# Kernel optimization log

Hardware: AMD Instinct MI355X
Metric: run time of the kernel (lower is better)

The kernel has to match this reference:

```python
import jax, jax.numpy as jnp
import numpy as np

B, L, D_MODEL = 2, 1024, 1024
N_LAYERS = 2
D_INNER = 2 * D_MODEL          # expand = 2
D_STATE = 16
D_CONV = 4
DT_RANK = (D_MODEL + 15) // 16  # ceil(d_model/16) = 64
INIT_SCALE = 0.02


def setup_inputs() -> dict:
    key = jax.random.key(0)
    ks = jax.random.split(key, 8)
    f32 = jnp.float32
    dt_init = float(np.log(np.expm1(0.01)))  # softplus^-1(0.01), standard mamba dt bias init
    return {
        "x": jax.random.normal(ks[0], (B, L, D_MODEL), f32),
        "W_in": jax.random.normal(ks[1], (N_LAYERS, 2 * D_INNER, D_MODEL), f32) * INIT_SCALE,
        "conv_w": jax.random.normal(ks[2], (N_LAYERS, D_INNER, D_CONV), f32) * INIT_SCALE,
        "conv_b": jnp.zeros((N_LAYERS, D_INNER), f32),
        "W_x": jax.random.normal(ks[3], (N_LAYERS, DT_RANK + 2 * D_STATE, D_INNER), f32) * INIT_SCALE,
        "W_dt": jax.random.normal(ks[4], (N_LAYERS, D_INNER, DT_RANK), f32) * INIT_SCALE,
        "b_dt": jnp.full((N_LAYERS, D_INNER), dt_init, f32),
        "A_log": jnp.tile(jnp.log(jnp.arange(1, D_STATE + 1, dtype=f32)), (N_LAYERS, D_INNER, 1)),
        "D": jnp.ones((N_LAYERS, D_INNER), f32),
        "W_out": jax.random.normal(ks[5], (N_LAYERS, D_MODEL, D_INNER), f32) * INIT_SCALE,
    }


def _silu(x):
    return x * jax.nn.sigmoid(x)


def _causal_conv1d(u, w, b):
    # u: [B, L, D_INNER], w: [D_INNER, D_CONV] depthwise, b: [D_INNER]
    ut = jnp.pad(jnp.transpose(u, (0, 2, 1)), ((0, 0), (0, 0), (D_CONV - 1, 0)))
    y = jax.lax.conv_general_dilated(
        ut, w[:, None, :], window_strides=(1,), padding='VALID',
        feature_group_count=D_INNER, dimension_numbers=('NCH', 'OIH', 'NCH'))
    return jnp.transpose(y + b[None, :, None], (0, 2, 1))


def _selective_scan(u, dt, A, Bm, Cm, Dvec):
    # u, dt: [B, L, D_INNER]; A: [D_INNER, N]; Bm, Cm: [B, L, N]; Dvec: [D_INNER]
    dA = jnp.exp(dt[..., None] * A)                        # [B,L,Din,N]
    dBu = dt[..., None] * Bm[:, :, None, :] * u[..., None]  # [B,L,Din,N]

    def step(h, xs):
        dA_t, dBu_t, C_t = xs                              # [B,Din,N],[B,Din,N],[B,N]
        h = dA_t * h + dBu_t
        y = jnp.einsum('bdn,bn->bd', h, C_t)
        return h, y

    h0 = jnp.zeros((u.shape[0], D_INNER, D_STATE), u.dtype)
    _, ys = jax.lax.scan(step, h0, (jnp.swapaxes(dA, 0, 1),
                                    jnp.swapaxes(dBu, 0, 1),
                                    jnp.swapaxes(Cm, 0, 1)))
    return jnp.swapaxes(ys, 0, 1) + u * Dvec               # [B,L,Din]


def _mamba_layer(x, W_in, conv_w, conv_b, W_x, W_dt, b_dt, A_log, Dvec, W_out):
    xz = jnp.einsum('bld,ed->ble', x, W_in)                # [B,L,2*Din]
    u, z = jnp.split(xz, 2, axis=-1)
    u = _silu(_causal_conv1d(u, conv_w, conv_b))
    x_dbl = jnp.einsum('bld,rd->blr', u, W_x)              # [B,L,dt_rank+2N]
    dt, Bm, Cm = jnp.split(x_dbl, [DT_RANK, DT_RANK + D_STATE], axis=-1)
    dt = jax.nn.softplus(jnp.einsum('blr,dr->bld', dt, W_dt) + b_dt)
    A = -jnp.exp(A_log)
    y = _selective_scan(u, dt, A, Bm, Cm, Dvec)
    y = y * _silu(z)
    return jnp.einsum('bld,od->blo', y, W_out)


def reference(x, W_in, conv_w, conv_b, W_x, W_dt, b_dt, A_log, D, W_out):
    residual = x
    h = x
    for i in range(N_LAYERS):
        h = _mamba_layer(h, W_in[i], conv_w[i], conv_b[i], W_x[i],
                         W_dt[i], b_dt[i], A_log[i], D[i], W_out[i])
    return h + residual
```

## Files before the change

### kernel.cpp

```cpp
#include <hip/hip_runtime.h>
#include <hip/hip_bf16.h>
#include <math.h>

#define B_ 2
#define L_ 1024
#define DM 1024
#define DIN 2048
#define DS 16
#define DTR 64
#define CHL 32
#define NCH 32

typedef __attribute__((ext_vector_type(8))) short bf16x8;
typedef __attribute__((ext_vector_type(8))) unsigned short u16x8;
typedef __attribute__((ext_vector_type(4))) unsigned short u16x4;
typedef __attribute__((ext_vector_type(4))) float f32x4;
typedef unsigned short ushort_t;
typedef unsigned int uint_t;

__device__ __forceinline__ float sigmoidf_(float x) { return 1.f / (1.f + __expf(-x)); }
__device__ __forceinline__ ushort_t f2b(float f) {
    uint_t b = __float_as_uint(f);
    return (ushort_t)((b + 0x7FFFu + ((b >> 16) & 1u)) >> 16);
}
__device__ __forceinline__ float b2f(ushort_t u) {
    return __uint_as_float(((uint_t)u) << 16);
}

__global__ __launch_bounds__(256) void f2b_all_k(
    const float* __restrict__ s0, ushort_t* __restrict__ d0, int n0,
    const float* __restrict__ s1, ushort_t* __restrict__ d1, int n1,
    const float* __restrict__ s2, ushort_t* __restrict__ d2, int n2,
    const float* __restrict__ s3, ushort_t* __restrict__ d3, int n3,
    const float* __restrict__ s4, ushort_t* __restrict__ d4, int n4)
{
    int i = (blockIdx.x * 256 + threadIdx.x) * 4;
    const float* s; ushort_t* d;
    if (i < n0) { s = s0; d = d0; }
    else { i -= n0;
    if (i < n1) { s = s1; d = d1; }
    else { i -= n1;
    if (i < n2) { s = s2; d = d2; }
    else { i -= n2;
    if (i < n3) { s = s3; d = d3; }
    else { i -= n3;
    if (i < n4) { s = s4; d = d4; }
    else return; }}}}
    float4 v = *(const float4*)(s + i);
    u16x4 o;
    o[0] = f2b(v.x); o[1] = f2b(v.y); o[2] = f2b(v.z); o[3] = f2b(v.w);
    *(u16x4*)(d + i) = o;
}

__device__ __forceinline__ int xcd_swz(int wgid, int nwg) {
    int cpx = nwg >> 3;
    return (wgid & 7) * cpx + (wgid >> 3);
}

__global__ __launch_bounds__(256) void mgemm_in(const ushort_t* __restrict__ A,
    const ushort_t* __restrict__ Bt, ushort_t* __restrict__ Cb,
    int M, int N, int K, int lda, int ldb)
{
    __shared__ ushort_t sA[2][128 * 32];
    __shared__ ushort_t sB[2][128 * 32];
    const int tid = threadIdx.x;
    const int lane = tid & 63, wv = tid >> 6;
    const int wm = wv >> 1, wn = wv & 1;
    const int swz = xcd_swz(blockIdx.y * gridDim.x + blockIdx.x, gridDim.x * gridDim.y);
    const int m0 = (swz / gridDim.x) * 128, n0 = (swz % gridDim.x) * 128;
    const int sr = tid >> 2;
    const int sc = (tid & 3) * 8;
    f32x4 acc[4][4] = {};

#pragma unroll
    for (int j = 0; j < 2; ++j) {
        int ra = sr + j * 64;
        __builtin_amdgcn_global_load_lds(
            (const uint_t*)(A + (size_t)(m0 + ra) * lda + sc),
            (uint_t*)(sA[0] + ra * 32 + sc), 16, 0, 0);
        __builtin_amdgcn_global_load_lds(
            (const uint_t*)(Bt + (size_t)(n0 + ra) * ldb + sc),
            (uint_t*)(sB[0] + ra * 32 + sc), 16, 0, 0);
    }
    __syncthreads();
    int cur = 0;
    for (int k0 = 0; k0 < K; k0 += 32) {
        if (k0 + 32 < K) {
            int nxt = cur ^ 1;
#pragma unroll
            for (int j = 0; j < 2; ++j) {
                int ra = sr + j * 64;
                __builtin_amdgcn_global_load_lds(
                    (const uint_t*)(A + (size_t)(m0 + ra) * lda + k0 + 32 + sc),
                    (uint_t*)(sA[nxt] + ra * 32 + sc), 16, 0, 0);
                __builtin_amdgcn_global_load_lds(
                    (const uint_t*)(Bt + (size_t)(n0 + ra) * ldb + k0 + 32 + sc),
                    (uint_t*)(sB[nxt] + ra * 32 + sc), 16, 0, 0);
            }
        }
        bf16x8 af[4], bfr[4];
#pragma unroll
        for (int i = 0; i < 4; ++i) {
            af[i]  = *(const bf16x8*)(sA[cur] + (wm * 64 + i * 16 + (lane & 15)) * 32 + (lane >> 4) * 8);
            bfr[i] = *(const bf16x8*)(sB[cur] + (wn * 64 + i * 16 + (lane & 15)) * 32 + (lane >> 4) * 8);
        }
#pragma unroll
        for (int i = 0; i < 4; ++i)
#pragma unroll
            for (int jj = 0; jj < 4; ++jj)
                acc[i][jj] = __builtin_amdgcn_mfma_f32_16x16x32_bf16(af[i], bfr[jj], acc[i][jj], 0, 0, 0);
        __syncthreads();
        cur ^= 1;
    }

    const int cr = (lane >> 4) * 4, cc = lane & 15;
#pragma unroll
    for (int i = 0; i < 4; ++i) {
        int mrow = m0 + wm * 64 + i * 16 + cr;
#pragma unroll
        for (int jj = 0; jj < 4; ++jj) {
            int ncol = n0 + wn * 64 + jj * 16 + cc;
#pragma unroll
            for (int r = 0; r < 4; ++r)
                Cb[(size_t)(mrow + r) * N + ncol] = f2b(acc[i][jj][r]);
        }
    }
}

__global__ __launch_bounds__(256) void mgemm_sk(const ushort_t* __restrict__ A,
    const ushort_t* __restrict__ Bt, float* __restrict__ P,
    int M, int N, int Kslice, int lda, int ldb)
{
    __shared__ ushort_t sA[2][128 * 32];
    __shared__ ushort_t sB[2][128 * 32];
    const int tid = threadIdx.x;
    const int lane = tid & 63, wv = tid >> 6;
    const int wm = wv >> 1, wn = wv & 1;
    const int m0 = blockIdx.y * 128;
    const int kbase = blockIdx.z * Kslice;
    const int sr = tid >> 2;
    const int sc = (tid & 3) * 8;
    f32x4 acc[4][4] = {};

#pragma unroll
    for (int j = 0; j < 2; ++j) {
        int ra = sr + j * 64;
        __builtin_amdgcn_global_load_lds(
            (const uint_t*)(A + (size_t)(m0 + ra) * lda + kbase + sc),
            (uint_t*)(sA[0] + ra * 32 + sc), 16, 0, 0);
        int gb = ra; if (gb >= N) gb = N - 1;
        __builtin_amdgcn_global_load_lds(
            (const uint_t*)(Bt + (size_t)gb * ldb + kbase + sc),
            (uint_t*)(sB[0] + ra * 32 + sc), 16, 0, 0);
    }
    __syncthreads();
    int cur = 0;
    for (int k0 = kbase; k0 < kbase + Kslice; k0 += 32) {
        if (k0 + 32 < kbase + Kslice) {
            int nxt = cur ^ 1;
#pragma unroll
            for (int j = 0; j < 2; ++j) {
                int ra = sr + j * 64;
                __builtin_amdgcn_global_load_lds(
                    (const uint_t*)(A + (size_t)(m0 + ra) * lda + k0 + 32 + sc),
                    (uint_t*)(sA[nxt] + ra * 32 + sc), 16, 0, 0);
                int gb = ra; if (gb >= N) gb = N - 1;
                __builtin_amdgcn_global_load_lds(
                    (const uint_t*)(Bt + (size_t)gb * ldb + k0 + 32 + sc),
                    (uint_t*)(sB[nxt] + ra * 32 + sc), 16, 0, 0);
            }
        }
        bf16x8 af[4], bfr[4];
#pragma unroll
        for (int i = 0; i < 4; ++i) {
            af[i]  = *(const bf16x8*)(sA[cur] + (wm * 64 + i * 16 + (lane & 15)) * 32 + (lane >> 4) * 8);
            bfr[i] = *(const bf16x8*)(sB[cur] + (wn * 64 + i * 16 + (lane & 15)) * 32 + (lane >> 4) * 8);
        }
#pragma unroll
        for (int i = 0; i < 4; ++i)
#pragma unroll
            for (int jj = 0; jj < 4; ++jj)
                acc[i][jj] = __builtin_amdgcn_mfma_f32_16x16x32_bf16(af[i], bfr[jj], acc[i][jj], 0, 0, 0);
        __syncthreads();
        cur ^= 1;
    }

    const int cr = (lane >> 4) * 4, cc = lane & 15;
    float* Pz = P + (size_t)blockIdx.z * M * 96;
#pragma unroll
    for (int i = 0; i < 4; ++i) {
        int mrow = m0 + wm * 64 + i * 16 + cr;
#pragma unroll
        for (int jj = 0; jj < 4; ++jj) {
            int ncol = wn * 64 + jj * 16 + cc;
            if (ncol < 96) {
#pragma unroll
                for (int r = 0; r < 4; ++r)
                    Pz[(size_t)(mrow + r) * 96 + ncol] = acc[i][jj][r];
            }
        }
    }
}

__global__ __launch_bounds__(256) void mgemm_dtf(const float* __restrict__ P,
    const ushort_t* __restrict__ Wd, const float* __restrict__ bias,
    float* __restrict__ xdbl, ushort_t* __restrict__ dtfb)
{
    __shared__ ushort_t sA[2][128 * 36];
    __shared__ ushort_t sB[2][128 * 32];
    const int tid = threadIdx.x;
    const int lane = tid & 63, wv = tid >> 6;
    const int wm = wv >> 1, wn = wv & 1;
    const int n0 = blockIdx.x * 128, m0 = blockIdx.y * 128;

#pragma unroll
    for (int kh = 0; kh < 2; ++kh)
#pragma unroll
        for (int it = 0; it < 2; ++it) {
            int ci = tid + it * 256;
            int row = ci >> 2, cc = ci & 3;
            __builtin_amdgcn_global_load_lds(
                (const uint_t*)(Wd + (size_t)(n0 + row) * 64 + kh * 32 + cc * 8),
                (uint_t*)(sB[kh] + (size_t)ci * 8), 16, 0, 0);
        }

#pragma unroll
    for (int it = 0; it < 8; ++it) {
        int ci = tid + it * 256;
        int row = ci >> 4, c4 = (ci & 15) * 4;
        float s0 = 0.f, s1 = 0.f, s2 = 0.f, s3 = 0.f;
#pragma unroll
        for (int z = 0; z < 8; ++z) {
            f32x4 v = *(const f32x4*)(P + (size_t)z * 196608 + (size_t)(m0 + row) * 96 + c4);
            s0 += v[0]; s1 += v[1]; s2 += v[2]; s3 += v[3];
        }
        u16x4 o; o[0] = f2b(s0); o[1] = f2b(s1); o[2] = f2b(s2); o[3] = f2b(s3);
        int kh = c4 >> 5, cl = c4 & 31;
        *(u16x4*)(sA[kh] + row * 36 + cl) = o;
    }
    if (blockIdx.x == 0) {
#pragma unroll
        for (int it = 0; it < 4; ++it) {
            int ci = tid + it * 256;
            int row = ci >> 3, c4 = (ci & 7) * 4;
            f32x4 s = {0.f, 0.f, 0.f, 0.f};
#pragma unroll
            for (int z = 0; z < 8; ++z) {
                f32x4 v = *(const f32x4*)(P + (size_t)z * 196608 + (size_t)(m0 + row) * 96 + 64 + c4);
                s[0] += v[0]; s[1] += v[1]; s[2] += v[2]; s[3] += v[3];
            }
            *(f32x4*)(xdbl + (size_t)(m0 + row) * 96 + 64 + c4) = s;
        }
    }
    __syncthreads();

    f32x4 acc[4][4] = {};
#pragma unroll
    for (int ks = 0; ks < 2; ++ks) {
        bf16x8 af[4], bfr[4];
#pragma unroll
        for (int i = 0; i < 4; ++i) {
            af[i]  = *(const bf16x8*)(sA[ks] + (wm * 64 + i * 16 + (lane & 15)) * 36 + (lane >> 4) * 8);
            bfr[i] = *(const bf16x8*)(sB[ks] + (wn * 64 + i * 16 + (lane & 15)) * 32 + (lane >> 4) * 8);
        }
#pragma unroll
        for (int i = 0; i < 4; ++i)
#pragma unroll
            for (int jj = 0; jj < 4; ++jj)
                acc[i][jj] = __builtin_amdgcn_mfma_f32_16x16x32_bf16(af[i], bfr[jj], acc[i][jj], 0, 0, 0);
    }

    const int cr = (lane >> 4) * 4, cc = lane & 15;
#pragma unroll
    for (int i = 0; i < 4; ++i) {
        int mrow = m0 + wm * 64 + i * 16 + cr;
#pragma unroll
        for (int jj = 0; jj < 4; ++jj) {
            int ncol = n0 + wn * 64 + jj * 16 + cc;
#pragma unroll
            for (int r = 0; r < 4; ++r) {
                float s = acc[i][jj][r] + bias[ncol];
                dtfb[(size_t)(mrow + r) * DIN + ncol] =
                    f2b((s > 20.f) ? s : log1pf(expf(s)));
            }
        }
    }
}

template<int EPI>
__global__ __launch_bounds__(256) void mgemm_n64(const ushort_t* __restrict__ A,
    const ushort_t* __restrict__ Bt, float* __restrict__ Cf, ushort_t* __restrict__ Cb,
    const float* __restrict__ res, int M, int N, int K, int lda, int ldb)
{
    __shared__ ushort_t sA[2][128 * 32];
    __shared__ ushort_t sB[2][64 * 32];
    const int tid = threadIdx.x;
    const int lane = tid & 63, wv = tid >> 6;
    const int swz = xcd_swz(blockIdx.y * gridDim.x + blockIdx.x, gridDim.x * gridDim.y);
    const int m0 = (swz / gridDim.x) * 128, n0 = (swz % gridDim.x) * 64;
    const int sr = tid >> 2;
    const int sc = (tid & 3) * 8;
    f32x4 acc[2][4] = {};

#pragma unroll
    for (int j = 0; j < 2; ++j) {
        int ra = sr + j * 64;
        __builtin_amdgcn_global_load_lds(
            (const uint_t*)(A + (size_t)(m0 + ra) * lda + sc),
            (uint_t*)(sA[0] + ra * 32 + sc), 16, 0, 0);
    }
    __builtin_amdgcn_global_load_lds(
        (const uint_t*)(Bt + (size_t)(n0 + sr) * ldb + sc),
        (uint_t*)(sB[0] + sr * 32 + sc), 16, 0, 0);
    __syncthreads();
    int cur = 0;
    for (int k0 = 0; k0 < K; k0 += 32) {
        if (k0 + 32 < K) {
            int nxt = cur ^ 1;
#pragma unroll
            for (int j = 0; j < 2; ++j) {
                int ra = sr + j * 64;
                __builtin_amdgcn_global_load_lds(
                    (const uint_t*)(A + (size_t)(m0 + ra) * lda + k0 + 32 + sc),
                    (uint_t*)(sA[nxt] + ra * 32 + sc), 16, 0, 0);
            }
            __builtin_amdgcn_global_load_lds(
                (const uint_t*)(Bt + (size_t)(n0 + sr) * ldb + k0 + 32 + sc),
                (uint_t*)(sB[nxt] + sr * 32 + sc), 16, 0, 0);
        }
        bf16x8 af[2], bfr[4];
#pragma unroll
        for (int i = 0; i < 2; ++i)
            af[i]  = *(const bf16x8*)(sA[cur] + (wv * 32 + i * 16 + (lane & 15)) * 32 + (lane >> 4) * 8);
#pragma unroll
        for (int jj = 0; jj < 4; ++jj)
            bfr[jj] = *(const bf16x8*)(sB[cur] + (jj * 16 + (lane & 15)) * 32 + (lane >> 4) * 8);
#pragma unroll
        for (int i = 0; i < 2; ++i)
#pragma unroll
            for (int jj = 0; jj < 4; ++jj)
                acc[i][jj] = __builtin_amdgcn_mfma_f32_16x16x32_bf16(af[i], bfr[jj], acc[i][jj], 0, 0, 0);
        __syncthreads();
        cur ^= 1;
    }

    const int cr = (lane >> 4) * 4, cc = lane & 15;
#pragma unroll
    for (int i = 0; i < 2; ++i) {
        int mrow = m0 + wv * 32 + i * 16 + cr;
#pragma unroll
        for (int jj = 0; jj < 4; ++jj) {
            int ncol = n0 + jj * 16 + cc;
#pragma unroll
            for (int r = 0; r < 4; ++r) {
                float v = acc[i][jj][r];
                size_t off = (size_t)(mrow + r) * N + ncol;
                if (EPI == 3) Cb[off] = f2b(v);
                else Cf[off] = v + res[off];
            }
        }
    }
}

__global__ __launch_bounds__(256) void conv8_k(const ushort_t* __restrict__ xzb,
    const float* __restrict__ cw, const float* __restrict__ cb,
    ushort_t* __restrict__ ucb)
{
    int idx8 = blockIdx.x * 256 + threadIdx.x;
    int d8 = (idx8 & 255) * 8;
    int t = (idx8 >> 8) & (L_ - 1);
    int b = idx8 >> 18;
    const ushort_t* base = xzb + (size_t)b * L_ * (2 * DIN) + d8;
    float acc[8];
    const float4* cb4 = (const float4*)(cb + d8);
    float4 cbl = cb4[0], cbh = cb4[1];
#pragma unroll
    for (int e = 0; e < 4; ++e) { acc[e] = ((const float*)&cbl)[e]; acc[4 + e] = ((const float*)&cbh)[e]; }
    float4 cwv[8];
#pragma unroll
    for (int e = 0; e < 8; ++e) cwv[e] = ((const float4*)cw)[d8 + e];
#pragma unroll
    for (int j = 0; j < 4; ++j) {
        int tt = t - 3 + j;
        if (tt >= 0) {
            u16x8 row = *(const u16x8*)(base + (size_t)tt * (2 * DIN));
#pragma unroll
            for (int e = 0; e < 8; ++e)
                acc[e] = fmaf(((const float*)&cwv[e])[j], b2f(row[e]), acc[e]);
        }
    }
    u16x8 ob;
#pragma unroll
    for (int e = 0; e < 8; ++e) {
        float v = acc[e] * sigmoidf_(acc[e]);
        ob[e] = f2b(v);
    }
    *(u16x8*)(ucb + (size_t)idx8 * 8) = ob;
}

__global__ __launch_bounds__(256, 2) void scan_s1(const ushort_t* __restrict__ dtfb,
    const ushort_t* __restrict__ ucb, const float* __restrict__ xdbl,
    const float* __restrict__ A_log,
    float* __restrict__ bnd_q, float* __restrict__ bnd_s)
{
    __shared__ uint_t sdt[CHL * 256];
    __shared__ float sB[CHL * 16];
    const int tid = threadIdx.x;
    const int bx = blockIdx.x;
    const int dg = bx & 7, c = (bx >> 3) & 31, b = bx >> 8;
    const int d = dg * 256 + tid;
    const int row0 = b * L_ + c * CHL;

    float A_dn[16];
#pragma unroll
    for (int n = 0; n < 16; ++n) A_dn[n] = -__expf(A_log[(size_t)d * DS + n]);

    for (int k = 0; k < CHL; ++k) {
        size_t off = (size_t)(row0 + k) * DIN + d;
        sdt[k * 256 + tid] = (uint_t)dtfb[off] | ((uint_t)ucb[off] << 16);
    }
#pragma unroll
    for (int j = 0; j < 2; ++j) {
        int idx = tid + j * 256;
        int t = idx >> 4, n = idx & 15;
        sB[idx] = xdbl[(size_t)(row0 + t) * 96 + 64 + n];
    }
    __syncthreads();

    float q[16];
#pragma unroll
    for (int n = 0; n < 16; ++n) q[n] = 0.f;
    float s = 0.f;
    for (int k = 0; k < CHL; ++k) {
        uint_t pk = sdt[k * 256 + tid];
        float dtv = __uint_as_float(pk << 16);
        float uv  = __uint_as_float(pk & 0xffff0000u);
        float dtu = dtv * uv;
        s += dtv;
        f32x4 Bq[4];
#pragma unroll
        for (int j = 0; j < 4; ++j) Bq[j] = *(const f32x4*)(sB + k * 16 + j * 4);
#pragma unroll
        for (int n = 0; n < 16; ++n)
            q[n] = fmaf(__expf(dtv * A_dn[n]), q[n], dtu * Bq[n >> 2][n & 3]);
    }
    float* qp = bnd_q + ((size_t)(b * NCH + c) * DIN + d) * 16;
#pragma unroll
    for (int j = 0; j < 4; ++j)
        *(f32x4*)(qp + j * 4) = (f32x4){q[j * 4], q[j * 4 + 1], q[j * 4 + 2], q[j * 4 + 3]};
    bnd_s[(size_t)(b * NCH + c) * DIN + d] = s;
}

__global__ __launch_bounds__(256, 2) void scan_s2(const ushort_t* __restrict__ dtfb,
    const ushort_t* __restrict__ ucb_in, const float* __restrict__ xdbl,
    const ushort_t* __restrict__ xzb, const float* __restrict__ A_log,
    const float* __restrict__ Dvec, const float* __restrict__ bnd_q,
    const float* __restrict__ bnd_s, ushort_t* __restrict__ ucb_out)
{
    __shared__ uint_t sdt[CHL * 256];
    __shared__ float sBC[CHL * 32];
    const int tid = threadIdx.x;
    const int bx = blockIdx.x;
    const int dg = bx & 7, c = (bx >> 3) & 31, b = bx >> 8;
    const int d = dg * 256 + tid;
    const int row0 = b * L_ + c * CHL;
    const float Dd = Dvec[d];

    float A_dn[16];
#pragma unroll
    for (int n = 0; n < 16; ++n) A_dn[n] = -__expf(A_log[(size_t)d * DS + n]);

    for (int k = 0; k < CHL; ++k) {
        size_t off = (size_t)(row0 + k) * DIN + d;
        sdt[k * 256 + tid] = (uint_t)dtfb[off] | ((uint_t)ucb_in[off] << 16);
    }
#pragma unroll
    for (int j = 0; j < 4; ++j) {
        int idx = tid + j * 256;
        int t = idx >> 5, jj = idx & 31;
        sBC[idx] = xdbl[(size_t)(row0 + t) * 96 + 64 + (jj & 1) * 16 + (jj >> 1)];
    }

    float h[16];
#pragma unroll
    for (int n = 0; n < 16; ++n) h[n] = 0.f;
    const size_t cb_base = (size_t)b * NCH * DIN + d;
    for (int cc = 0; cc < c; ++cc) {
        size_t idx = cb_base + (size_t)cc * DIN;
        float sv = bnd_s[idx];
        const float* qp = bnd_q + idx * 16;
        f32x4 qv[4];
#pragma unroll
        for (int j = 0; j < 4; ++j) qv[j] = *(const f32x4*)(qp + j * 4);
#pragma unroll
        for (int n = 0; n < 16; ++n)
            h[n] = fmaf(__expf(A_dn[n] * sv), h[n], qv[n >> 2][n & 3]);
    }
    __syncthreads();

    for (int k = 0; k < CHL; ++k) {
        uint_t pk = sdt[k * 256 + tid];
        float dtv = __uint_as_float(pk << 16);
        float uv  = __uint_as_float(pk & 0xffff0000u);
        float dtu = dtv * uv;
        float z = b2f(xzb[(size_t)(row0 + k) * (2 * DIN) + DIN + d]);
        float y = uv * Dd;
        f32x4 bcq[8];
#pragma unroll
        for (int j = 0; j < 8; ++j) bcq[j] = *(const f32x4*)(sBC + k * 32 + j * 4);
#pragma unroll
        for (int n = 0; n < 16; ++n) {
            float Bv = bcq[n >> 1][(n & 1) * 2];
            float Cv = bcq[n >> 1][(n & 1) * 2 + 1];
            h[n] = fmaf(__expf(dtv * A_dn[n]), h[n], dtu * Bv);
            y = fmaf(h[n], Cv, y);
        }
        y *= z * sigmoidf_(z);
        ucb_out[(size_t)(row0 + k) * DIN + d] = f2b(y);
    }
}

extern "C" void kernel_launch(void* const* d_in, const int* in_sizes, int n_in,
                              void* d_out, int out_size, void* d_ws, size_t ws_size,
                              hipStream_t stream)
{
    (void)in_sizes; (void)n_in; (void)out_size; (void)ws_size;
    const float* x      = (const float*)d_in[0];
    const float* W_in   = (const float*)d_in[1];
    const float* conv_w = (const float*)d_in[2];
    const float* conv_b = (const float*)d_in[3];
    const float* W_x    = (const float*)d_in[4];
    const float* W_dt   = (const float*)d_in[5];
    const float* b_dt   = (const float*)d_in[6];
    const float* A_log  = (const float*)d_in[7];
    const float* Dv     = (const float*)d_in[8];
    const float* W_out  = (const float*)d_in[9];
    float* out = (float*)d_out;

    float* xdbl    = (float*)d_ws;
    float* pws     = xdbl + 196608;
    float* bnd_q   = pws + 1572864;
    float* bnd_s   = bnd_q + 2097152;
    ushort_t* dtfb = (ushort_t*)(bnd_s + 131072);
    ushort_t* xzb  = dtfb + 4194304;
    ushort_t* ucb  = xzb + 8388608;
    ushort_t* xb   = ucb + 4194304;
    ushort_t* wib  = xb + 2097152;
    ushort_t* wxb  = wib + 8388608;
    ushort_t* wdb  = wxb + 393216;
    ushort_t* wob  = wdb + 262144;

    const int M = B_ * L_;
    const int NT = 2097152 + 8388608 + 393216 + 262144 + 4194304;
    f2b_all_k<<<(NT / 4) / 256, 256, 0, stream>>>(
        x, xb, 2097152, W_in, wib, 8388608, W_x, wxb, 393216,
        W_dt, wdb, 262144, W_out, wob, 4194304);

    for (int layer = 0; layer < 2; ++layer) {
        mgemm_in<<<dim3(4096 / 128, M / 128), 256, 0, stream>>>(
            xb, wib + (size_t)layer * 4194304, xzb, M, 2 * DIN, DM, DM, DM);
        conv8_k<<<(B_ * L_ * DIN / 8) / 256, 256, 0, stream>>>(
            xzb, conv_w + (size_t)layer * DIN * 4, conv_b + (size_t)layer * DIN, ucb);
        mgemm_sk<<<dim3(1, M / 128, 8), 256, 0, stream>>>(
            ucb, wxb + (size_t)layer * 196608, pws, M, 96, DIN / 8, DIN, DIN);
        mgemm_dtf<<<dim3(16, 16), 256, 0, stream>>>(
            pws, wdb + (size_t)layer * 131072, b_dt + (size_t)layer * DIN, xdbl, dtfb);
        const float* Al = A_log + (size_t)layer * DIN * DS;
        scan_s1<<<B_ * NCH * 8, 256, 0, stream>>>(dtfb, ucb, xdbl, Al, bnd_q, bnd_s);
        scan_s2<<<B_ * NCH * 8, 256, 0, stream>>>(dtfb, ucb, xdbl, xzb, Al,
            Dv + (size_t)layer * DIN, bnd_q, bnd_s, ucb);
        if (layer == 0)
            mgemm_n64<3><<<dim3(1024 / 64, M / 128), 256, 0, stream>>>(
                ucb, wob + (size_t)layer * 2097152, nullptr, xb, nullptr,
                M, DM, DIN, DIN, DIN);
        else
            mgemm_n64<4><<<dim3(1024 / 64, M / 128), 256, 0, stream>>>(
                ucb, wob + (size_t)layer * 2097152, out, nullptr, x,
                M, DM, DIN, DIN, DIN);
    }
}
```

Measured before the change: 451.1 us.

## Split-K output projection and stage scan inputs via async LDS loads

The output GEMM now runs as a 2-way split-K kernel that writes fp32 partials to workspace, followed by a small reduction kernel that adds the partials, applies the residual or bf16 conversion, and writes the result. The aim is to double the block count and fill more CUs. Both scan kernels now load dt, u and z tiles into LDS with 16-byte global_load_lds copies instead of per-thread scalar loads. scan_s2 also stages its outputs in LDS and writes them back as coalesced 16-byte stores. The cost is an extra kernel launch plus extra fp32 partial traffic, and the XCD swizzle was removed from the output GEMM.

```diff
diff --git a/kernel.cpp b/kernel.cpp
--- a/kernel.cpp
+++ b/kernel.cpp
@@ -287,17 +287,16 @@
     }
 }
 
-template<int EPI>
-__global__ __launch_bounds__(256) void mgemm_n64(const ushort_t* __restrict__ A,
-    const ushort_t* __restrict__ Bt, float* __restrict__ Cf, ushort_t* __restrict__ Cb,
-    const float* __restrict__ res, int M, int N, int K, int lda, int ldb)
+__global__ __launch_bounds__(256) void mgemm_o(const ushort_t* __restrict__ A,
+    const ushort_t* __restrict__ Bt, float* __restrict__ P,
+    int M, int N, int Kslice, int lda, int ldb)
 {
     __shared__ ushort_t sA[2][128 * 32];
     __shared__ ushort_t sB[2][64 * 32];
     const int tid = threadIdx.x;
     const int lane = tid & 63, wv = tid >> 6;
-    const int swz = xcd_swz(blockIdx.y * gridDim.x + blockIdx.x, gridDim.x * gridDim.y);
-    const int m0 = (swz / gridDim.x) * 128, n0 = (swz % gridDim.x) * 64;
+    const int m0 = blockIdx.y * 128, n0 = blockIdx.x * 64;
+    const int kbase = blockIdx.z * Kslice;
     const int sr = tid >> 2;
     const int sc = (tid & 3) * 8;
     f32x4 acc[2][4] = {};
@@ -306,16 +305,16 @@
     for (int j = 0; j < 2; ++j) {
         int ra = sr + j * 64;
         __builtin_amdgcn_global_load_lds(
-            (const uint_t*)(A + (size_t)(m0 + ra) * lda + sc),
+            (const uint_t*)(A + (size_t)(m0 + ra) * lda + kbase + sc),
             (uint_t*)(sA[0] + ra * 32 + sc), 16, 0, 0);
     }
     __builtin_amdgcn_global_load_lds(
-        (const uint_t*)(Bt + (size_t)(n0 + sr) * ldb + sc),
+        (const uint_t*)(Bt + (size_t)(n0 + sr) * ldb + kbase + sc),
         (uint_t*)(sB[0] + sr * 32 + sc), 16, 0, 0);
     __syncthreads();
     int cur = 0;
-    for (int k0 = 0; k0 < K; k0 += 32) {
-        if (k0 + 32 < K) {
+    for (int k0 = kbase; k0 < kbase + Kslice; k0 += 32) {
+        if (k0 + 32 < kbase + Kslice) {
             int nxt = cur ^ 1;
 #pragma unroll
             for (int j = 0; j < 2; ++j) {
@@ -345,6 +344,7 @@
     }
 
     const int cr = (lane >> 4) * 4, cc = lane & 15;
+    float* Pz = P + (size_t)blockIdx.z * M * DM;
 #pragma unroll
     for (int i = 0; i < 2; ++i) {
         int mrow = m0 + wv * 32 + i * 16 + cr;
@@ -352,13 +352,30 @@
         for (int jj = 0; jj < 4; ++jj) {
             int ncol = n0 + jj * 16 + cc;
 #pragma unroll
-            for (int r = 0; r < 4; ++r) {
-                float v = acc[i][jj][r];
-                size_t off = (size_t)(mrow + r) * N + ncol;
-                if (EPI == 3) Cb[off] = f2b(v);
-                else Cf[off] = v + res[off];
-            }
-        }
+            for (int r = 0; r < 4; ++r)
+                Pz[(size_t)(mrow + r) * DM + ncol] = acc[i][jj][r];
+        }
+    }
+}
+
+template<int EPI>
+__global__ __launch_bounds__(256) void ored_k(const float* __restrict__ P,
+    const float* __restrict__ res, float* __restrict__ Cf, ushort_t* __restrict__ Cb)
+{
+    int i = (blockIdx.x * 256 + threadIdx.x) * 4;
+    f32x4 a = *(const f32x4*)(P + i);
+    f32x4 b = *(const f32x4*)(P + 2097152 + i);
+    if (EPI == 3) {
+        u16x4 o;
+#pragma unroll
+        for (int e = 0; e < 4; ++e) o[e] = f2b(a[e] + b[e]);
+        *(u16x4*)(Cb + i) = o;
+    } else {
+        f32x4 r = *(const f32x4*)(res + i);
+        f32x4 o;
+#pragma unroll
+        for (int e = 0; e < 4; ++e) o[e] = a[e] + b[e] + r[e];
+        *(f32x4*)(Cf + i) = o;
     }
 }
 
@@ -403,21 +420,29 @@
     const float* __restrict__ A_log,
     float* __restrict__ bnd_q, float* __restrict__ bnd_s)
 {
-    __shared__ uint_t sdt[CHL * 256];
+    __shared__ ushort_t s_dt[CHL * 256];
+    __shared__ ushort_t s_u[CHL * 256];
     __shared__ float sB[CHL * 16];
     const int tid = threadIdx.x;
     const int bx = blockIdx.x;
     const int dg = bx & 7, c = (bx >> 3) & 31, b = bx >> 8;
     const int d = dg * 256 + tid;
+    const int dbase = dg * 256;
     const int row0 = b * L_ + c * CHL;
 
     float A_dn[16];
 #pragma unroll
     for (int n = 0; n < 16; ++n) A_dn[n] = -__expf(A_log[(size_t)d * DS + n]);
 
-    for (int k = 0; k < CHL; ++k) {
-        size_t off = (size_t)(row0 + k) * DIN + d;
-        sdt[k * 256 + tid] = (uint_t)dtfb[off] | ((uint_t)ucb[off] << 16);
+    const int rr = tid >> 5, c16 = (tid & 31) * 8;
+#pragma unroll
+    for (int it = 0; it < 4; ++it) {
+        int k = rr + it * 8;
+        size_t gro = (size_t)(row0 + k) * DIN + dbase + c16;
+        __builtin_amdgcn_global_load_lds((const uint_t*)(dtfb + gro),
+            (uint_t*)(s_dt + k * 256 + c16), 16, 0, 0);
+        __builtin_amdgcn_global_load_lds((const uint_t*)(ucb + gro),
+            (uint_t*)(s_u + k * 256 + c16), 16, 0, 0);
     }
 #pragma unroll
     for (int j = 0; j < 2; ++j) {
@@ -432,9 +457,8 @@
     for (int n = 0; n < 16; ++n) q[n] = 0.f;
     float s = 0.f;
     for (int k = 0; k < CHL; ++k) {
-        uint_t pk = sdt[k * 256 + tid];
-        float dtv = __uint_as_float(pk << 16);
-        float uv  = __uint_as_float(pk & 0xffff0000u);
+        float dtv = b2f(s_dt[k * 256 + tid]);
+        float uv  = b2f(s_u[k * 256 + tid]);
         float dtu = dtv * uv;
         s += dtv;
         f32x4 Bq[4];
@@ -457,12 +481,15 @@
     const float* __restrict__ Dvec, const float* __restrict__ bnd_q,
     const float* __restrict__ bnd_s, ushort_t* __restrict__ ucb_out)
 {
-    __shared__ uint_t sdt[CHL * 256];
+    __shared__ ushort_t s_dt[CHL * 256];
+    __shared__ ushort_t s_u[CHL * 256];
+    __shared__ ushort_t s_z[CHL * 256];
     __shared__ float sBC[CHL * 32];
     const int tid = threadIdx.x;
     const int bx = blockIdx.x;
     const int dg = bx & 7, c = (bx >> 3) & 31, b = bx >> 8;
     const int d = dg * 256 + tid;
+    const int dbase = dg * 256;
     const int row0 = b * L_ + c * CHL;
     const float Dd = Dvec[d];
 
@@ -470,9 +497,18 @@
 #pragma unroll
     for (int n = 0; n < 16; ++n) A_dn[n] = -__expf(A_log[(size_t)d * DS + n]);
 
-    for (int k = 0; k < CHL; ++k) {
-        size_t off = (size_t)(row0 + k) * DIN + d;
-        sdt[k * 256 + tid] = (uint_t)dtfb[off] | ((uint_t)ucb_in[off] << 16);
+    const int rr = tid >> 5, c16 = (tid & 31) * 8;
+#pragma unroll
+    for (int it = 0; it < 4; ++it) {
+        int k = rr + it * 8;
+        size_t gro = (size_t)(row0 + k) * DIN + dbase + c16;
+        __builtin_amdgcn_global_load_lds((const uint_t*)(dtfb + gro),
+            (uint_t*)(s_dt + k * 256 + c16), 16, 0, 0);
+        __builtin_amdgcn_global_load_lds((const uint_t*)(ucb_in + gro),
+            (uint_t*)(s_u + k * 256 + c16), 16, 0, 0);
+        __builtin_amdgcn_global_load_lds(
+            (const uint_t*)(xzb + (size_t)(row0 + k) * (2 * DIN) + DIN + dbase + c16),
+            (uint_t*)(s_z + k * 256 + c16), 16, 0, 0);
     }
 #pragma unroll
     for (int j = 0; j < 4; ++j) {
@@ -499,11 +535,10 @@
     __syncthreads();
 
     for (int k = 0; k < CHL; ++k) {
-        uint_t pk = sdt[k * 256 + tid];
-        float dtv = __uint_as_float(pk << 16);
-        float uv  = __uint_as_float(pk & 0xffff0000u);
+        float dtv = b2f(s_dt[k * 256 + tid]);
+        float uv  = b2f(s_u[k * 256 + tid]);
+        float z   = b2f(s_z[k * 256 + tid]);
         float dtu = dtv * uv;
-        float z = b2f(xzb[(size_t)(row0 + k) * (2 * DIN) + DIN + d]);
         float y = uv * Dd;
         f32x4 bcq[8];
 #pragma unroll
@@ -516,7 +551,14 @@
             y = fmaf(h[n], Cv, y);
         }
         y *= z * sigmoidf_(z);
-        ucb_out[(size_t)(row0 + k) * DIN + d] = f2b(y);
+        s_dt[k * 256 + tid] = f2b(y);
+    }
+    __syncthreads();
+#pragma unroll
+    for (int it = 0; it < 4; ++it) {
+        int k = rr + it * 8;
+        *(u16x8*)(ucb_out + (size_t)(row0 + k) * DIN + dbase + c16) =
+            *(const u16x8*)(s_dt + k * 256 + c16);
     }
 }
 
@@ -549,6 +591,7 @@
     ushort_t* wxb  = wib + 8388608;
     ushort_t* wdb  = wxb + 393216;
     ushort_t* wob  = wdb + 262144;
+    float* pwo     = (float*)(wob + 4194304);
 
     const int M = B_ * L_;
     const int NT = 2097152 + 8388608 + 393216 + 262144 + 4194304;
@@ -569,13 +612,11 @@
         scan_s1<<<B_ * NCH * 8, 256, 0, stream>>>(dtfb, ucb, xdbl, Al, bnd_q, bnd_s);
         scan_s2<<<B_ * NCH * 8, 256, 0, stream>>>(dtfb, ucb, xdbl, xzb, Al,
             Dv + (size_t)layer * DIN, bnd_q, bnd_s, ucb);
+        mgemm_o<<<dim3(1024 / 64, M / 128, 2), 256, 0, stream>>>(
+            ucb, wob + (size_t)layer * 2097152, pwo, M, DM, DIN / 2, DIN, DIN);
         if (layer == 0)
-            mgemm_n64<3><<<dim3(1024 / 64, M / 128), 256, 0, stream>>>(
-                ucb, wob + (size_t)layer * 2097152, nullptr, xb, nullptr,
-                M, DM, DIN, DIN, DIN);
+            ored_k<3><<<(2097152 / 4) / 256, 256, 0, stream>>>(pwo, nullptr, nullptr, xb);
         else
-            mgemm_n64<4><<<dim3(1024 / 64, M / 128), 256, 0, stream>>>(
-                ucb, wob + (size_t)layer * 2097152, out, nullptr, x,
-                M, DM, DIN, DIN, DIN);
-    }
-}
+            ored_k<4><<<(2097152 / 4) / 256, 256, 0, stream>>>(pwo, x, out, nullptr);
+    }
+}
```

Result: faster. 436.5 us (-3.2%).
